# Performance work log

Hardware: AMD Instinct MI355X
Metric: run time of the kernel (lower is better)

The kernel has to match this reference:

```python
import math
import jax, jax.numpy as jnp
import numpy as np

B, S, E, H = 4, 2048, 1024, 16
HD = E // H  # 64


def setup_inputs() -> dict:
    key = jax.random.key(0)
    ks = jax.random.split(key, 7)
    scale = 1.0 / math.sqrt(E)
    return {
        "x": jax.random.normal(ks[0], (B, S, E), dtype=jnp.float32),
        "Wq": jax.random.normal(ks[1], (H, HD, E), dtype=jnp.float32) * scale,
        "bq": jax.random.normal(ks[2], (H, HD), dtype=jnp.float32) * 0.01,
        "Wk": jax.random.normal(ks[3], (H, HD, E), dtype=jnp.float32) * scale,
        "bk": jax.random.normal(ks[4], (H, HD), dtype=jnp.float32) * 0.01,
        "Wv": jax.random.normal(ks[5], (H, HD, E), dtype=jnp.float32) * scale,
        "bv": jax.random.normal(ks[6], (H, HD), dtype=jnp.float32) * 0.01,
    }


def reference(x, Wq, bq, Wk, bk, Wv, bv):
    b, s, e = x.shape
    h, hd, _ = Wq.shape
    inv_scale = 1.0 / math.sqrt(hd)
    # per-head linear projections (torch Linear: x @ W^T + b), batched over heads
    q = jnp.einsum("bse,hde->bshd", x, Wq) + bq  # [B,S,H,HD]
    k = jnp.einsum("bse,hde->bshd", x, Wk) + bk
    v = jnp.einsum("bse,hde->bshd", x, Wv) + bv
    # causal mask: -inf above diagonal (added before scaling, as in source;
    # -inf * inv_scale is still -inf so math is identical)
    mask = jnp.triu(jnp.full((s, s), -jnp.inf, dtype=x.dtype), k=1)
    scores = (jnp.einsum("bqhd,bkhd->bhqk", q, k) + mask) * inv_scale  # [B,H,S,S]
    attn = jax.nn.softmax(scores, axis=-1)
    out = jnp.einsum("bhqk,bkhd->bqhd", attn, v)  # [B,S,H,HD]
    # concat over heads in head order == reshape with head-major last dims
    return out.reshape(b, s, h * hd)
```

## Files before the change

### kernel.cpp

```cpp
#include <hip/hip_runtime.h>


typedef __bf16 bf16x8 __attribute__((ext_vector_type(8)));
typedef __bf16 bf16x4 __attribute__((ext_vector_type(4)));
typedef float f32x4 __attribute__((ext_vector_type(4)));
typedef unsigned short us8 __attribute__((ext_vector_type(8)));
typedef unsigned short us4 __attribute__((ext_vector_type(4)));

#define Bb 4
#define Ss 2048
#define Ee 1024
#define Hh 16
#define HD 64

#if __has_builtin(__builtin_amdgcn_exp2f)
#define EXP2(x) __builtin_amdgcn_exp2f(x)
#else
#define EXP2(x) exp2f(x)
#endif

__device__ __forceinline__ unsigned short f2bf(float f) {
  union { float f; unsigned u; } v; v.f = f;
  unsigned u = v.u;
  u += 0x7fffu + ((u >> 16) & 1u);
  return (unsigned short)(u >> 16);
}

__device__ __forceinline__ void gl_lds16(const void* g, void* l) {
  __builtin_amdgcn_global_load_lds((const __attribute__((address_space(1))) void*)g,
                                   (__attribute__((address_space(3))) void*)l, 16, 0, 0);
}

#define DSR(d, a, o) asm volatile("ds_read_b128 %0, %1 offset:" #o : "=v"(d) : "v"(a))

__global__ __launch_bounds__(256) void cvt_all(const float* __restrict__ x,
                                               const float* __restrict__ wq,
                                               const float* __restrict__ wk,
                                               const float* __restrict__ wv,
                                               unsigned short* __restrict__ xb,
                                               unsigned short* __restrict__ wb) {
  int i = blockIdx.x * 256 + threadIdx.x;
  const float* src; unsigned short* dst; int idx;
  if (i < 2097152)      { src = x;  dst = xb;                idx = i; }
  else if (i < 2359296) { src = wq; dst = wb;                idx = i - 2097152; }
  else if (i < 2621440) { src = wk; dst = wb + 1048576;      idx = i - 2359296; }
  else                  { src = wv; dst = wb + 2 * 1048576;  idx = i - 2621440; }
  float4 f = ((const float4*)src)[idx];
  us4 o = { f2bf(f.x), f2bf(f.y), f2bf(f.z), f2bf(f.w) };
  ((us4*)dst)[idx] = o;
}

__global__ __launch_bounds__(512, 2) void qkv_gemm(const unsigned short* __restrict__ xb,
                                                   const unsigned short* __restrict__ wb_all,
                                                   const float* __restrict__ bq,
                                                   const float* __restrict__ bk,
                                                   const float* __restrict__ bv,
                                                   unsigned short* __restrict__ qkv) {
  const int z = blockIdx.z;
  const unsigned short* wb = wb_all + (size_t)z * (Ee * Ee);
  const float* bias = (z == 0) ? bq : (z == 1) ? bk : bv;
  unsigned short* outb = qkv + (size_t)z * (Bb * Ss * Ee);
  const float osc = (z == 0) ? 0.180336880f : 1.0f;

  __shared__ unsigned short SMEM[65536];

  const int t = threadIdx.x;
  const int wave = t >> 6, lane = t & 63, quad = lane >> 4, ln = lane & 15;
  const int wr = wave >> 2, wc = wave & 3;
  const int m0 = blockIdx.x * 256, n0 = blockIdx.y * 256;

  const int r8 = t >> 3;
  const int cs = ((t & 7) ^ (r8 & 7)) * 8;
  const int t8 = t * 8;
  const unsigned short* gA0 = xb + (size_t)(m0 + r8) * Ee + cs;
  const unsigned short* gA1 = gA0 + 128 * Ee;
  const unsigned short* gB0 = wb + (size_t)(n0 + r8) * Ee + cs;
  const unsigned short* gB1 = gB0 + 128 * Ee;

  const int swz0 = ((0 * 4 + quad) ^ (ln & 7)) * 16;
  const int swz1 = ((1 * 4 + quad) ^ (ln & 7)) * 16;
  int aA0 = (wr * 64 + ln) * 128 + swz0;
  int aA1 = (wr * 64 + ln) * 128 + swz1;
  int bA0 = 32768 + (wc * 32 + ln) * 128 + swz0;
  int bA1 = 32768 + (wc * 32 + ln) * 128 + swz1;

  f32x4 acc[2][2][4][2] = {};
  bf16x8 af[4][2], bf0[2][2], bf1[2][2];

  gl_lds16(gA0,           &SMEM[t8]);
  gl_lds16(gA0 + 64 * Ee, &SMEM[t8 + 4096]);
  gl_lds16(gB0,           &SMEM[16384 + t8]);
  gl_lds16(gB0 + 64 * Ee, &SMEM[16384 + t8 + 4096]);
  gl_lds16(gB1,           &SMEM[24576 + t8]);
  gl_lds16(gB1 + 64 * Ee, &SMEM[24576 + t8 + 4096]);
  gl_lds16(gA1,           &SMEM[8192 + t8]);
  gl_lds16(gA1 + 64 * Ee, &SMEM[8192 + t8 + 4096]);

#pragma unroll 1
  for (int kt = 0; kt < 15; ++kt) {
    const int sbuf = ((kt & 1) << 15) ^ 32768;
    const int co = (kt + 1) * 64;

    asm volatile("s_waitcnt vmcnt(4)" ::: "memory");
    asm volatile("s_barrier" ::: "memory");
    DSR(af[0][0], aA0, 0);    DSR(af[1][0], aA0, 2048);
    DSR(af[2][0], aA0, 4096); DSR(af[3][0], aA0, 6144);
    DSR(af[0][1], aA1, 0);    DSR(af[1][1], aA1, 2048);
    DSR(af[2][1], aA1, 4096); DSR(af[3][1], aA1, 6144);
    DSR(bf0[0][0], bA0, 0);   DSR(bf0[1][0], bA0, 2048);
    DSR(bf0[0][1], bA1, 0);   DSR(bf0[1][1], bA1, 2048);
    gl_lds16(gA0 + co,           &SMEM[sbuf + t8]);
    gl_lds16(gA0 + co + 64 * Ee, &SMEM[sbuf + t8 + 4096]);
    asm volatile("s_barrier" ::: "memory");
    asm volatile("s_waitcnt lgkmcnt(0)" ::: "memory");
    __builtin_amdgcn_sched_barrier(0);
    __builtin_amdgcn_s_setprio(1);
#pragma unroll
    for (int kk = 0; kk < 2; ++kk)
#pragma unroll
      for (int i = 0; i < 4; ++i)
#pragma unroll
        for (int j = 0; j < 2; ++j)
          acc[0][0][i][j] = __builtin_amdgcn_mfma_f32_16x16x32_bf16(af[i][kk], bf0[j][kk], acc[0][0][i][j], 0, 0, 0);
    __builtin_amdgcn_s_setprio(0);
    __builtin_amdgcn_sched_barrier(0);

    asm volatile("s_waitcnt vmcnt(4)" ::: "memory");
    asm volatile("s_barrier" ::: "memory");
    DSR(bf1[0][0], bA0, 16384); DSR(bf1[1][0], bA0, 18432);
    DSR(bf1[0][1], bA1, 16384); DSR(bf1[1][1], bA1, 18432);
    gl_lds16(gB0 + co,           &SMEM[sbuf + 16384 + t8]);
    gl_lds16(gB0 + co + 64 * Ee, &SMEM[sbuf + 16384 + t8 + 4096]);
    asm volatile("s_barrier" ::: "memory");
    asm volatile("s_waitcnt lgkmcnt(0)" ::: "memory");
    __builtin_amdgcn_sched_barrier(0);
    __builtin_amdgcn_s_setprio(1);
#pragma unroll
    for (int kk = 0; kk < 2; ++kk)
#pragma unroll
      for (int i = 0; i < 4; ++i)
#pragma unroll
        for (int j = 0; j < 2; ++j)
          acc[0][1][i][j] = __builtin_amdgcn_mfma_f32_16x16x32_bf16(af[i][kk], bf1[j][kk], acc[0][1][i][j], 0, 0, 0);
    __builtin_amdgcn_s_setprio(0);
    __builtin_amdgcn_sched_barrier(0);

    asm volatile("s_waitcnt vmcnt(4)" ::: "memory");
    asm volatile("s_barrier" ::: "memory");
    DSR(af[0][0], aA0, 16384); DSR(af[1][0], aA0, 18432);
    DSR(af[2][0], aA0, 20480); DSR(af[3][0], aA0, 22528);
    DSR(af[0][1], aA1, 16384); DSR(af[1][1], aA1, 18432);
    DSR(af[2][1], aA1, 20480); DSR(af[3][1], aA1, 22528);
    gl_lds16(gB1 + co,           &SMEM[sbuf + 24576 + t8]);
    gl_lds16(gB1 + co + 64 * Ee, &SMEM[sbuf + 24576 + t8 + 4096]);
    asm volatile("s_barrier" ::: "memory");
    asm volatile("s_waitcnt lgkmcnt(0)" ::: "memory");
    __builtin_amdgcn_sched_barrier(0);
    __builtin_amdgcn_s_setprio(1);
#pragma unroll
    for (int kk = 0; kk < 2; ++kk)
#pragma unroll
      for (int i = 0; i < 4; ++i)
#pragma unroll
        for (int j = 0; j < 2; ++j)
          acc[1][0][i][j] = __builtin_amdgcn_mfma_f32_16x16x32_bf16(af[i][kk], bf0[j][kk], acc[1][0][i][j], 0, 0, 0);
    __builtin_amdgcn_s_setprio(0);
    __builtin_amdgcn_sched_barrier(0);

    asm volatile("s_barrier" ::: "memory");
    gl_lds16(gA1 + co,           &SMEM[sbuf + 8192 + t8]);
    gl_lds16(gA1 + co + 64 * Ee, &SMEM[sbuf + 8192 + t8 + 4096]);
    asm volatile("s_barrier" ::: "memory");
    __builtin_amdgcn_sched_barrier(0);
    __builtin_amdgcn_s_setprio(1);
#pragma unroll
    for (int kk = 0; kk < 2; ++kk)
#pragma unroll
      for (int i = 0; i < 4; ++i)
#pragma unroll
        for (int j = 0; j < 2; ++j)
          acc[1][1][i][j] = __builtin_amdgcn_mfma_f32_16x16x32_bf16(af[i][kk], bf1[j][kk], acc[1][1][i][j], 0, 0, 0);
    __builtin_amdgcn_s_setprio(0);
    __builtin_amdgcn_sched_barrier(0);

    aA0 ^= 65536; aA1 ^= 65536; bA0 ^= 65536; bA1 ^= 65536;
  }

  {
    asm volatile("s_waitcnt vmcnt(0)" ::: "memory");
    asm volatile("s_barrier" ::: "memory");
    DSR(af[0][0], aA0, 0);    DSR(af[1][0], aA0, 2048);
    DSR(af[2][0], aA0, 4096); DSR(af[3][0], aA0, 6144);
    DSR(af[0][1], aA1, 0);    DSR(af[1][1], aA1, 2048);
    DSR(af[2][1], aA1, 4096); DSR(af[3][1], aA1, 6144);
    DSR(bf0[0][0], bA0, 0);   DSR(bf0[1][0], bA0, 2048);
    DSR(bf0[0][1], bA1, 0);   DSR(bf0[1][1], bA1, 2048);
    DSR(bf1[0][0], bA0, 16384); DSR(bf1[1][0], bA0, 18432);
    DSR(bf1[0][1], bA1, 16384); DSR(bf1[1][1], bA1, 18432);
    asm volatile("s_waitcnt lgkmcnt(0)" ::: "memory");
    __builtin_amdgcn_sched_barrier(0);
#pragma unroll
    for (int kk = 0; kk < 2; ++kk)
#pragma unroll
      for (int i = 0; i < 4; ++i)
#pragma unroll
        for (int j = 0; j < 2; ++j) {
          acc[0][0][i][j] = __builtin_amdgcn_mfma_f32_16x16x32_bf16(af[i][kk], bf0[j][kk], acc[0][0][i][j], 0, 0, 0);
          acc[0][1][i][j] = __builtin_amdgcn_mfma_f32_16x16x32_bf16(af[i][kk], bf1[j][kk], acc[0][1][i][j], 0, 0, 0);
        }
    __builtin_amdgcn_sched_barrier(0);
    DSR(af[0][0], aA0, 16384); DSR(af[1][0], aA0, 18432);
    DSR(af[2][0], aA0, 20480); DSR(af[3][0], aA0, 22528);
    DSR(af[0][1], aA1, 16384); DSR(af[1][1], aA1, 18432);
    DSR(af[2][1], aA1, 20480); DSR(af[3][1], aA1, 22528);
    asm volatile("s_waitcnt lgkmcnt(0)" ::: "memory");
    __builtin_amdgcn_sched_barrier(0);
#pragma unroll
    for (int kk = 0; kk < 2; ++kk)
#pragma unroll
      for (int i = 0; i < 4; ++i)
#pragma unroll
        for (int j = 0; j < 2; ++j) {
          acc[1][0][i][j] = __builtin_amdgcn_mfma_f32_16x16x32_bf16(af[i][kk], bf0[j][kk], acc[1][0][i][j], 0, 0, 0);
          acc[1][1][i][j] = __builtin_amdgcn_mfma_f32_16x16x32_bf16(af[i][kk], bf1[j][kk], acc[1][1][i][j], 0, 0, 0);
        }
    __builtin_amdgcn_sched_barrier(0);
  }

  float biasj[2][2];
#pragma unroll
  for (int qb = 0; qb < 2; ++qb)
#pragma unroll
    for (int j = 0; j < 2; ++j)
      biasj[qb][j] = bias[n0 + qb * 128 + wc * 32 + j * 16 + ln];

  if (z != 2) {
#pragma unroll
    for (int qa = 0; qa < 2; ++qa)
#pragma unroll
      for (int qb = 0; qb < 2; ++qb)
#pragma unroll
        for (int i = 0; i < 4; ++i)
#pragma unroll
          for (int j = 0; j < 2; ++j)
#pragma unroll
            for (int r = 0; r < 4; ++r) {
              int m = m0 + qa * 128 + wr * 64 + i * 16 + quad * 4 + r;
              int n = n0 + qb * 128 + wc * 32 + j * 16 + ln;
              int b_ = m >> 11, s = m & 2047;
              int h = n >> 6, d = n & 63;
              outb[(((size_t)b_ * Hh + h) * Ss + s) * HD + d] =
                  f2bf((acc[qa][qb][i][j][r] + biasj[qb][j]) * osc);
            }
  } else {
    for (int qa = 0; qa < 2; ++qa) {
      __syncthreads();
#pragma unroll
      for (int qb = 0; qb < 2; ++qb)
#pragma unroll
        for (int i = 0; i < 4; ++i)
#pragma unroll
          for (int j = 0; j < 2; ++j)
#pragma unroll
            for (int r = 0; r < 4; ++r) {
              int nc = qb * 128 + wc * 32 + j * 16 + ln;
              int mr = wr * 64 + i * 16 + quad * 4 + r;
              SMEM[nc * 136 + mr] = f2bf(acc[qa][qb][i][j][r] + biasj[qb][j]);
            }
      __syncthreads();
      int nr = t >> 1, mh = t & 1;
      int n = n0 + nr, h = n >> 6, d = n & 63;
      int b_ = m0 >> 11;
      int s0 = (m0 & 2047) + qa * 128 + mh * 64;
#pragma unroll
      for (int q = 0; q < 8; ++q) {
        us8 vdat = *(const us8*)&SMEM[nr * 136 + mh * 64 + q * 8];
        *(us8*)&outb[(((size_t)b_ * Hh + h) * HD + d) * Ss + s0 + q * 8] = vdat;
      }
    }
  }
}

__global__ __launch_bounds__(256, 2) void flash_attn(const unsigned short* __restrict__ qkv,
                                                     float* __restrict__ out) {
  const int id = blockIdx.x;
  const int bh = id & 63;
  const int p = id >> 6;
  const int b_ = bh >> 4, h = bh & 15;

  const unsigned short* qb  = qkv + (size_t)bh * (Ss * HD);
  const unsigned short* kb  = qkv + (size_t)(64 + bh) * (Ss * HD);
  const unsigned short* vtb = qkv + (size_t)(128 + bh) * (Ss * HD);

  __shared__ __bf16 Ks[8192];
  __shared__ __bf16 Vt[8192];
  __shared__ __bf16 Ps[4][16][72];

  const int t = threadIdx.x;
  const int wave = t >> 6, lane = t & 63, quad = lane >> 4, ln = lane & 15;

  const int rk = t >> 3;
  const int ck = ((t & 7) ^ (rk & 7)) * 8;
  const int rv = t >> 4;
  const int cv = ((t & 15) ^ (rv & 7)) * 8;
  const int t8 = t * 8;

  const int qts[2] = { 15 - p, p };
  const int KTB = qts[0] + 1;

  bf16x8 qf[2][2][2];
#pragma unroll
  for (int qt = 0; qt < 2; ++qt)
#pragma unroll
    for (int u = 0; u < 2; ++u)
#pragma unroll
      for (int ks = 0; ks < 2; ++ks)
        qf[qt][u][ks] = *(const bf16x8*)(qb + (size_t)(qts[qt] * 128 + u * 64 + wave * 16 + ln) * HD +
                                         ks * 32 + quad * 8);

  bf16x8 onef;
#pragma unroll
  for (int j = 0; j < 8; ++j) onef[j] = (__bf16)1.0f;

  f32x4 o[2][2][4] = {};
  f32x4 l4[2][2] = {};

#pragma unroll 1
  for (int kt = 0; kt < KTB; ++kt) {
    const unsigned short* kbt = kb + (size_t)kt * (128 * HD);
    const unsigned short* vbt = vtb + kt * 128;
    __syncthreads();
    gl_lds16(kbt + rk * HD + ck,        &Ks[t8]);
    gl_lds16(kbt + (rk + 32) * HD + ck, &Ks[t8 + 2048]);
    gl_lds16(kbt + (rk + 64) * HD + ck, &Ks[t8 + 4096]);
    gl_lds16(kbt + (rk + 96) * HD + ck, &Ks[t8 + 6144]);
    gl_lds16(vbt + rv * Ss + cv,        &Vt[t8]);
    gl_lds16(vbt + (rv + 16) * Ss + cv, &Vt[t8 + 2048]);
    gl_lds16(vbt + (rv + 32) * Ss + cv, &Vt[t8 + 4096]);
    gl_lds16(vbt + (rv + 48) * Ss + cv, &Vt[t8 + 6144]);
    __syncthreads();

#pragma unroll
    for (int h2 = 0; h2 < 2; ++h2) {
      const int kb64 = kt * 2 + h2;
#pragma unroll
      for (int qt = 0; qt < 2; ++qt) {
        const int qtp = qts[qt];
#pragma unroll
        for (int u = 0; u < 2; ++u) {
          const int su = 2 * qtp + u;
          if (kb64 > su) continue;
          const int qrow = qtp * 128 + u * 64 + wave * 16 + ln;

          f32x4 s_acc[4] = {};
#pragma unroll
          for (int g = 0; g < 4; ++g)
#pragma unroll
            for (int ks = 0; ks < 2; ++ks) {
              bf16x8 kf = *(const bf16x8*)&Ks[(h2 * 64 + g * 16 + ln) * 64 +
                                              (((ks * 4 + quad) ^ (ln & 7)) * 8)];
              s_acc[g] = __builtin_amdgcn_mfma_f32_16x16x32_bf16(kf, qf[qt][u][ks], s_acc[g], 0, 0, 0);
            }

          if (kb64 == su) {
            const int k0 = kb64 * 64;
#pragma unroll
            for (int g = 0; g < 4; ++g)
#pragma unroll
              for (int r = 0; r < 4; ++r) {
                int kcol = k0 + g * 16 + quad * 4 + r;
                if (kcol > qrow) s_acc[g][r] = -__builtin_inff();
              }
          }

#pragma unroll
          for (int g = 0; g < 4; ++g) {
            bf16x4 pk = { (__bf16)EXP2(s_acc[g][0]), (__bf16)EXP2(s_acc[g][1]),
                          (__bf16)EXP2(s_acc[g][2]), (__bf16)EXP2(s_acc[g][3]) };
            *(bf16x4*)&Ps[wave][ln][g * 16 + quad * 4] = pk;
          }
          bf16x8 pf[2];
#pragma unroll
          for (int ks = 0; ks < 2; ++ks)
            pf[ks] = *(const bf16x8*)&Ps[wave][ln][ks * 32 + quad * 8];

          l4[qt][u] = __builtin_amdgcn_mfma_f32_16x16x32_bf16(pf[0], onef, l4[qt][u], 0, 0, 0);
          l4[qt][u] = __builtin_amdgcn_mfma_f32_16x16x32_bf16(pf[1], onef, l4[qt][u], 0, 0, 0);

#pragma unroll
          for (int g = 0; g < 4; ++g)
#pragma unroll
            for (int ks = 0; ks < 2; ++ks) {
              bf16x8 vf = *(const bf16x8*)&Vt[(g * 16 + ln) * 128 +
                                              (((h2 * 8 + ks * 4 + quad) ^ (ln & 7)) * 8)];
              o[qt][u][g] = __builtin_amdgcn_mfma_f32_16x16x32_bf16(pf[ks], vf, o[qt][u][g], 0, 0, 0);
            }
        }
      }
    }
  }

#pragma unroll
  for (int qt = 0; qt < 2; ++qt)
#pragma unroll
    for (int u = 0; u < 2; ++u) {
      float linv[4];
#pragma unroll
      for (int r = 0; r < 4; ++r) linv[r] = 1.0f / l4[qt][u][r];
#pragma unroll
      for (int g = 0; g < 4; ++g)
#pragma unroll
        for (int r = 0; r < 4; ++r) {
          int orow = qts[qt] * 128 + u * 64 + wave * 16 + quad * 4 + r;
          out[((size_t)b_ * Ss + orow) * Ee + h * HD + g * 16 + ln] = o[qt][u][g][r] * linv[r];
        }
    }
}

extern "C" void kernel_launch(void* const* d_in, const int* in_sizes, int n_in,
                              void* d_out, int out_size, void* d_ws, size_t ws_size,
                              hipStream_t stream) {
  const float* x  = (const float*)d_in[0];
  const float* Wq = (const float*)d_in[1];
  const float* bq = (const float*)d_in[2];
  const float* Wk = (const float*)d_in[3];
  const float* bk = (const float*)d_in[4];
  const float* Wv = (const float*)d_in[5];
  const float* bv = (const float*)d_in[6];
  float* out = (float*)d_out;

  unsigned short* ws  = (unsigned short*)d_ws;
  unsigned short* xb  = ws;
  unsigned short* wb  = ws + 8388608;
  unsigned short* qkv = ws + 8388608 + 3 * 1048576;

  cvt_all<<<11264, 256, 0, stream>>>(x, Wq, Wk, Wv, xb, wb);
  qkv_gemm<<<dim3(32, 4, 3), 512, 0, stream>>>(xb, wb, bq, bk, bv, qkv);
  flash_attn<<<512, 256, 0, stream>>>(qkv, out);
}
```

Measured before the change: 213.5 us.

## Double flash-attention block to 8 waves sharing K/V tiles across four query tiles

The attention kernel now runs 256 blocks of 512 threads instead of 512 blocks of 256 threads. Each block processes four query tiles (p, 7-p, 8+p, 15-p) with the same staged K/V tile. The two wave halves take the two 64-row halves of each tile, so each K/V tile is loaded into shared memory once for twice as many query rows. This cuts global-to-LDS traffic and per-block load instructions, and the tile pairing keeps causal work equal across blocks. The cost is one block per CU with a larger barrier group, so stalls at __syncthreads may be harder to hide.

New measurement: 219.3 us. 2.7% more time.

```diff
diff --git a/kernel.cpp b/kernel.cpp
--- a/kernel.cpp
+++ b/kernel.cpp
@@ -281,11 +281,11 @@
   }
 }
 
-__global__ __launch_bounds__(256, 2) void flash_attn(const unsigned short* __restrict__ qkv,
+__global__ __launch_bounds__(512, 2) void flash_attn(const unsigned short* __restrict__ qkv,
                                                      float* __restrict__ out) {
   const int id = blockIdx.x;
-  const int bh = id & 63;
-  const int p = id >> 6;
+  const int bh = id >> 2;
+  const int p = id & 3;
   const int b_ = bh >> 4, h = bh & 15;
 
   const unsigned short* qb  = qkv + (size_t)bh * (Ss * HD);
@@ -294,10 +294,11 @@
 
   __shared__ __bf16 Ks[8192];
   __shared__ __bf16 Vt[8192];
-  __shared__ __bf16 Ps[4][16][72];
+  __shared__ __bf16 Ps[8][16][72];
 
   const int t = threadIdx.x;
   const int wave = t >> 6, lane = t & 63, quad = lane >> 4, ln = lane & 15;
+  const int uw = wave >> 2;
 
   const int rk = t >> 3;
   const int ck = ((t & 7) ^ (rk & 7)) * 8;
@@ -305,25 +306,23 @@
   const int cv = ((t & 15) ^ (rv & 7)) * 8;
   const int t8 = t * 8;
 
-  const int qts[2] = { 15 - p, p };
-  const int KTB = qts[0] + 1;
-
-  bf16x8 qf[2][2][2];
-#pragma unroll
-  for (int qt = 0; qt < 2; ++qt)
-#pragma unroll
-    for (int u = 0; u < 2; ++u)
-#pragma unroll
-      for (int ks = 0; ks < 2; ++ks)
-        qf[qt][u][ks] = *(const bf16x8*)(qb + (size_t)(qts[qt] * 128 + u * 64 + wave * 16 + ln) * HD +
-                                         ks * 32 + quad * 8);
+  const int qts[4] = { p, 7 - p, 8 + p, 15 - p };
+  const int KTB = 16 - p;
+
+  bf16x8 qf[4][2];
+#pragma unroll
+  for (int qt = 0; qt < 4; ++qt)
+#pragma unroll
+    for (int ks = 0; ks < 2; ++ks)
+      qf[qt][ks] = *(const bf16x8*)(qb + (size_t)(qts[qt] * 128 + wave * 16 + ln) * HD +
+                                    ks * 32 + quad * 8);
 
   bf16x8 onef;
 #pragma unroll
   for (int j = 0; j < 8; ++j) onef[j] = (__bf16)1.0f;
 
-  f32x4 o[2][2][4] = {};
-  f32x4 l4[2][2] = {};
+  f32x4 o[4][4] = {};
+  f32x4 l4[4] = {};
 
 #pragma unroll 1
   for (int kt = 0; kt < KTB; ++kt) {
@@ -331,90 +330,80 @@
     const unsigned short* vbt = vtb + kt * 128;
     __syncthreads();
     gl_lds16(kbt + rk * HD + ck,        &Ks[t8]);
-    gl_lds16(kbt + (rk + 32) * HD + ck, &Ks[t8 + 2048]);
     gl_lds16(kbt + (rk + 64) * HD + ck, &Ks[t8 + 4096]);
-    gl_lds16(kbt + (rk + 96) * HD + ck, &Ks[t8 + 6144]);
     gl_lds16(vbt + rv * Ss + cv,        &Vt[t8]);
-    gl_lds16(vbt + (rv + 16) * Ss + cv, &Vt[t8 + 2048]);
     gl_lds16(vbt + (rv + 32) * Ss + cv, &Vt[t8 + 4096]);
-    gl_lds16(vbt + (rv + 48) * Ss + cv, &Vt[t8 + 6144]);
     __syncthreads();
 
 #pragma unroll
     for (int h2 = 0; h2 < 2; ++h2) {
       const int kb64 = kt * 2 + h2;
 #pragma unroll
-      for (int qt = 0; qt < 2; ++qt) {
-        const int qtp = qts[qt];
-#pragma unroll
-        for (int u = 0; u < 2; ++u) {
-          const int su = 2 * qtp + u;
-          if (kb64 > su) continue;
-          const int qrow = qtp * 128 + u * 64 + wave * 16 + ln;
-
-          f32x4 s_acc[4] = {};
+      for (int qt = 0; qt < 4; ++qt) {
+        const int su = 2 * qts[qt] + uw;
+        if (kb64 > su) continue;
+        const int qrow = qts[qt] * 128 + wave * 16 + ln;
+
+        f32x4 s_acc[4] = {};
+#pragma unroll
+        for (int g = 0; g < 4; ++g)
+#pragma unroll
+          for (int ks = 0; ks < 2; ++ks) {
+            bf16x8 kf = *(const bf16x8*)&Ks[(h2 * 64 + g * 16 + ln) * 64 +
+                                            (((ks * 4 + quad) ^ (ln & 7)) * 8)];
+            s_acc[g] = __builtin_amdgcn_mfma_f32_16x16x32_bf16(kf, qf[qt][ks], s_acc[g], 0, 0, 0);
+          }
+
+        if (kb64 == su) {
+          const int k0 = kb64 * 64;
 #pragma unroll
           for (int g = 0; g < 4; ++g)
 #pragma unroll
-            for (int ks = 0; ks < 2; ++ks) {
-              bf16x8 kf = *(const bf16x8*)&Ks[(h2 * 64 + g * 16 + ln) * 64 +
-                                              (((ks * 4 + quad) ^ (ln & 7)) * 8)];
-              s_acc[g] = __builtin_amdgcn_mfma_f32_16x16x32_bf16(kf, qf[qt][u][ks], s_acc[g], 0, 0, 0);
-            }
-
-          if (kb64 == su) {
-            const int k0 = kb64 * 64;
-#pragma unroll
-            for (int g = 0; g < 4; ++g)
-#pragma unroll
-              for (int r = 0; r < 4; ++r) {
-                int kcol = k0 + g * 16 + quad * 4 + r;
-                if (kcol > qrow) s_acc[g][r] = -__builtin_inff();
-              }
-          }
-
-#pragma unroll
-          for (int g = 0; g < 4; ++g) {
-            bf16x4 pk = { (__bf16)EXP2(s_acc[g][0]), (__bf16)EXP2(s_acc[g][1]),
-                          (__bf16)EXP2(s_acc[g][2]), (__bf16)EXP2(s_acc[g][3]) };
-            *(bf16x4*)&Ps[wave][ln][g * 16 + quad * 4] = pk;
-          }
-          bf16x8 pf[2];
-#pragma unroll
-          for (int ks = 0; ks < 2; ++ks)
-            pf[ks] = *(const bf16x8*)&Ps[wave][ln][ks * 32 + quad * 8];
-
-          l4[qt][u] = __builtin_amdgcn_mfma_f32_16x16x32_bf16(pf[0], onef, l4[qt][u], 0, 0, 0);
-          l4[qt][u] = __builtin_amdgcn_mfma_f32_16x16x32_bf16(pf[1], onef, l4[qt][u], 0, 0, 0);
-
-#pragma unroll
-          for (int g = 0; g < 4; ++g)
-#pragma unroll
-            for (int ks = 0; ks < 2; ++ks) {
-              bf16x8 vf = *(const bf16x8*)&Vt[(g * 16 + ln) * 128 +
-                                              (((h2 * 8 + ks * 4 + quad) ^ (ln & 7)) * 8)];
-              o[qt][u][g] = __builtin_amdgcn_mfma_f32_16x16x32_bf16(pf[ks], vf, o[qt][u][g], 0, 0, 0);
+            for (int r = 0; r < 4; ++r) {
+              int kcol = k0 + g * 16 + quad * 4 + r;
+              if (kcol > qrow) s_acc[g][r] = -__builtin_inff();
             }
         }
+
+#pragma unroll
+        for (int g = 0; g < 4; ++g) {
+          bf16x4 pk = { (__bf16)EXP2(s_acc[g][0]), (__bf16)EXP2(s_acc[g][1]),
+                        (__bf16)EXP2(s_acc[g][2]), (__bf16)EXP2(s_acc[g][3]) };
+          *(bf16x4*)&Ps[wave][ln][g * 16 + quad * 4] = pk;
+        }
+        bf16x8 pf[2];
+#pragma unroll
+        for (int ks = 0; ks < 2; ++ks)
+          pf[ks] = *(const bf16x8*)&Ps[wave][ln][ks * 32 + quad * 8];
+
+        l4[qt] = __builtin_amdgcn_mfma_f32_16x16x32_bf16(pf[0], onef, l4[qt], 0, 0, 0);
+        l4[qt] = __builtin_amdgcn_mfma_f32_16x16x32_bf16(pf[1], onef, l4[qt], 0, 0, 0);
+
+#pragma unroll
+        for (int g = 0; g < 4; ++g)
+#pragma unroll
+          for (int ks = 0; ks < 2; ++ks) {
+            bf16x8 vf = *(const bf16x8*)&Vt[(g * 16 + ln) * 128 +
+                                            (((h2 * 8 + ks * 4 + quad) ^ (ln & 7)) * 8)];
+            o[qt][g] = __builtin_amdgcn_mfma_f32_16x16x32_bf16(pf[ks], vf, o[qt][g], 0, 0, 0);
+          }
       }
     }
   }
 
 #pragma unroll
-  for (int qt = 0; qt < 2; ++qt)
-#pragma unroll
-    for (int u = 0; u < 2; ++u) {
-      float linv[4];
-#pragma unroll
-      for (int r = 0; r < 4; ++r) linv[r] = 1.0f / l4[qt][u][r];
-#pragma unroll
-      for (int g = 0; g < 4; ++g)
-#pragma unroll
-        for (int r = 0; r < 4; ++r) {
-          int orow = qts[qt] * 128 + u * 64 + wave * 16 + quad * 4 + r;
-          out[((size_t)b_ * Ss + orow) * Ee + h * HD + g * 16 + ln] = o[qt][u][g][r] * linv[r];
-        }
-    }
+  for (int qt = 0; qt < 4; ++qt) {
+    float linv[4];
+#pragma unroll
+    for (int r = 0; r < 4; ++r) linv[r] = 1.0f / l4[qt][r];
+#pragma unroll
+    for (int g = 0; g < 4; ++g)
+#pragma unroll
+      for (int r = 0; r < 4; ++r) {
+        int orow = qts[qt] * 128 + wave * 16 + quad * 4 + r;
+        out[((size_t)b_ * Ss + orow) * Ee + h * HD + g * 16 + ln] = o[qt][g][r] * linv[r];
+      }
+  }
 }
 
 extern "C" void kernel_launch(void* const* d_in, const int* in_sizes, int n_in,
@@ -436,5 +425,5 @@
 
   cvt_all<<<11264, 256, 0, stream>>>(x, Wq, Wk, Wv, xb, wb);
   qkv_gemm<<<dim3(32, 4, 3), 512, 0, stream>>>(xb, wb, bq, bk, bv, qkv);
-  flash_attn<<<512, 256, 0, stream>>>(qkv, out);
-}
+  flash_attn<<<256, 512, 0, stream>>>(qkv, out);
+}
```
